# Kernel tuning notes

Hardware: AMD Instinct MI355X
Metric: run time of the kernel (lower is better)

Reference implementation:

```python
import jax, jax.numpy as jnp
import numpy as np
import math

D_MODEL = 1024
NUM_HEADS = 16
D_FF = 4096
EPS = 1e-5
BATCH = 2
SEQ = 2048


def _trunc_normal(key, shape, std):
    # truncated normal on [-3std, 3std], matching nn.init.trunc_normal_
    return std * jax.random.truncated_normal(key, -3.0, 3.0, shape, dtype=jnp.float32)


def setup_inputs() -> dict:
    key = jax.random.key(0)
    ks = jax.random.split(key, 8)
    x = jax.random.normal(ks[0], (BATCH, SEQ, D_MODEL), dtype=jnp.float32)
    std_dd = math.sqrt(2.0 / (D_MODEL + D_MODEL))
    std_up = math.sqrt(2.0 / (D_MODEL + D_FF))
    # Linear stores W as [out_features, in_features]; forward does x @ W.T
    W_q = _trunc_normal(ks[1], (D_MODEL, D_MODEL), std_dd)
    W_k = _trunc_normal(ks[2], (D_MODEL, D_MODEL), std_dd)
    W_v = _trunc_normal(ks[3], (D_MODEL, D_MODEL), std_dd)
    W_o = _trunc_normal(ks[4], (D_MODEL, D_MODEL), std_dd)
    W1 = _trunc_normal(ks[5], (D_FF, D_MODEL), std_up)
    W2 = _trunc_normal(ks[6], (D_MODEL, D_FF), std_up)
    ln1_w = jnp.ones((D_MODEL,), jnp.float32)
    ln1_b = jnp.zeros((D_MODEL,), jnp.float32)
    ln2_w = jnp.ones((D_MODEL,), jnp.float32)
    ln2_b = jnp.zeros((D_MODEL,), jnp.float32)
    return {"x": x, "W_q": W_q, "W_k": W_k, "W_v": W_v, "W_o": W_o,
            "W1": W1, "W2": W2,
            "ln1_w": ln1_w, "ln1_b": ln1_b, "ln2_w": ln2_w, "ln2_b": ln2_b}


def _layernorm(x, w, b):
    xf = x.astype(jnp.float32)
    mean = xf.mean(axis=-1, keepdims=True)
    var = jnp.mean((xf - mean) ** 2, axis=-1, keepdims=True)
    xn = (xf - mean) / jnp.sqrt(var + EPS)
    return (xn * w.astype(jnp.float32) + b.astype(jnp.float32)).astype(x.dtype)


def _attention(x, W_q, W_k, W_v, W_o):
    B, S, D = x.shape
    H, dk = NUM_HEADS, D // NUM_HEADS
    Q = (x @ W_q.T).reshape(B, S, H, dk).transpose(0, 2, 1, 3)  # [B,H,S,dk]
    K = (x @ W_k.T).reshape(B, S, H, dk).transpose(0, 2, 1, 3)
    V = (x @ W_v.T).reshape(B, S, H, dk).transpose(0, 2, 1, 3)
    scores = jnp.einsum('bhqd,bhkd->bhqk', Q, K) / math.sqrt(dk)
    causal = jnp.tril(jnp.ones((S, S), dtype=bool))
    scores = jnp.where(causal, scores, -jnp.inf)
    attn = jax.nn.softmax(scores, axis=-1)
    out = jnp.einsum('bhqk,bhkd->bhqd', attn, V)  # [B,H,S,dk]
    out = out.transpose(0, 2, 1, 3).reshape(B, S, D)
    return out @ W_o.T


def _ffn(x, W1, W2):
    h = x @ W1.T
    h = h * (h > 0)  # ReLU
    return h @ W2.T


def reference(x, W_q, W_k, W_v, W_o, W1, W2, ln1_w, ln1_b, ln2_w, ln2_b):
    x = x + _attention(_layernorm(x, ln1_w, ln1_b), W_q, W_k, W_v, W_o)
    x = x + _ffn(_layernorm(x, ln2_w, ln2_b), W1, W2)
    return x
```

## Files before the change

### kernel.cpp

```cpp
#include <hip/hip_runtime.h>
#include <stdint.h>

typedef unsigned short u16;
typedef unsigned int u32;
typedef __bf16 bf16x8 __attribute__((ext_vector_type(8)));
typedef float f32x4 __attribute__((ext_vector_type(4)));
typedef unsigned short u16x8 __attribute__((ext_vector_type(8)));
typedef unsigned short u16x4 __attribute__((ext_vector_type(4)));
typedef u16x8 u16x8_a __attribute__((may_alias));
typedef u16x4 u16x4_a __attribute__((may_alias));

#define DEV static __device__ __forceinline__

DEV u16 f2bf(float f) {
  unsigned u = __builtin_bit_cast(unsigned, f);
  u += 0x7fffu + ((u >> 16) & 1u);
  return (u16)(u >> 16);
}
DEV bf16x8 ld8(const u16* p) {
  u16x8 v = *(const u16x8_a*)p;
  return __builtin_bit_cast(bf16x8, v);
}
DEV f32x4 vmax4(f32x4 a, f32x4 b) {
  f32x4 r;
  r[0] = fmaxf(a[0], b[0]); r[1] = fmaxf(a[1], b[1]);
  r[2] = fmaxf(a[2], b[2]); r[3] = fmaxf(a[3], b[3]);
  return r;
}
DEV void swz_block(int& bx, int& by) {
  const int gx = gridDim.x;
  const int nwg = gx * gridDim.y;
  int lin = by * gx + bx;
  const int q = nwg >> 3, r = nwg & 7, x = lin & 7, p = lin >> 3;
  lin = (x < r ? x * (q + 1) : r * (q + 1) + (x - r) * q) + p;
  bx = lin % gx; by = lin / gx;
}

#define GL_LDS16(gp, lp)                                                        \
  __builtin_amdgcn_global_load_lds(                                             \
      (const __attribute__((address_space(1))) void*)(gp),                      \
      (__attribute__((address_space(3))) void*)(lp), 16, 0, 0)

#define VMW8 asm volatile("s_waitcnt vmcnt(8)" ::: "memory")
#define VMW4 asm volatile("s_waitcnt vmcnt(4)" ::: "memory")
#define VMW2 asm volatile("s_waitcnt vmcnt(2)" ::: "memory")
#define VMW0 asm volatile("s_waitcnt vmcnt(0)" ::: "memory")
#define BAR  __builtin_amdgcn_s_barrier()

__global__ __launch_bounds__(256) void cvt_k(const float* __restrict__ s,
                                             u16* __restrict__ d, int n4) {
  int i = blockIdx.x * 256 + threadIdx.x;
  if (i < n4) {
    float4 v = ((const float4*)s)[i];
    u16x4 o;
    o[0] = f2bf(v.x); o[1] = f2bf(v.y); o[2] = f2bf(v.z); o[3] = f2bf(v.w);
    *(u16x4_a*)(d + (size_t)i * 4) = o;
  }
}

__global__ __launch_bounds__(256) void ln_k(const float* __restrict__ x,
                                            const float* __restrict__ w,
                                            const float* __restrict__ b,
                                            u16* __restrict__ o) {
  const int row = blockIdx.x, t = threadIdx.x;
  const float4 v = ((const float4*)(x + (size_t)row * 1024))[t];
  float s = v.x + v.y + v.z + v.w;
  float q = v.x * v.x + v.y * v.y + v.z * v.z + v.w * v.w;
#pragma unroll
  for (int m = 1; m < 64; m <<= 1) { s += __shfl_xor(s, m); q += __shfl_xor(q, m); }
  __shared__ float ss[4], qq[4];
  if ((t & 63) == 0) { ss[t >> 6] = s; qq[t >> 6] = q; }
  __syncthreads();
  s = ss[0] + ss[1] + ss[2] + ss[3];
  q = qq[0] + qq[1] + qq[2] + qq[3];
  const float mean = s * (1.f / 1024.f);
  const float var = q * (1.f / 1024.f) - mean * mean;
  const float rstd = rsqrtf(var + 1e-5f);
  const float4 wv = ((const float4*)w)[t];
  const float4 bv = ((const float4*)b)[t];
  u16x4 ov;
  ov[0] = f2bf((v.x - mean) * rstd * wv.x + bv.x);
  ov[1] = f2bf((v.y - mean) * rstd * wv.y + bv.y);
  ov[2] = f2bf((v.z - mean) * rstd * wv.z + bv.z);
  ov[3] = f2bf((v.w - mean) * rstd * wv.w + bv.w);
  *(u16x4_a*)(o + (size_t)row * 1024 + t * 4) = ov;
}

__global__ __launch_bounds__(256) void vtr_k(const u16* __restrict__ qkvV,
                                             u16* __restrict__ vt) {
  __shared__ u16 T[64][65];
  const int st = blockIdx.x, bh = blockIdx.y;
  const int b = bh >> 4, h = bh & 15;
  const int t = threadIdx.x;
  const u16* src = qkvV + ((size_t)(b * 2048 + st * 64)) * 3072 + h * 64;
  const int r = t >> 2, c0 = (t & 3) * 16;
  u16x8 a0 = *(const u16x8_a*)(src + (size_t)r * 3072 + c0);
  u16x8 a1 = *(const u16x8_a*)(src + (size_t)r * 3072 + c0 + 8);
#pragma unroll
  for (int e = 0; e < 8; ++e) { T[r][c0 + e] = a0[e]; T[r][c0 + 8 + e] = a1[e]; }
  __syncthreads();
  const int d = t >> 2, s0 = (t & 3) * 16;
  u16x8 o0, o1;
#pragma unroll
  for (int e = 0; e < 8; ++e) { o0[e] = T[s0 + e][d]; o1[e] = T[s0 + 8 + e][d]; }
  u16* dst = vt + ((size_t)bh * 64 + d) * 2048 + (size_t)st * 64 + s0;
  *(u16x8_a*)dst = o0;
  *(u16x8_a*)(dst + 8) = o1;
}

DEV void stage_op(const u16* __restrict__ G, int K, int kk, u16* lds, int set,
                  int isB, int w, int l) {
#pragma unroll
  for (int i = 0; i < 2; ++i) {
    const int c = i * 8 + w;
    int rb;
    if (!isB) { const int lr = c * 8; rb = (lr < 64 ? lr : lr + 64) + set * 64; }
    else      { rb = (c >> 2) * 64 + set * 32 + (c & 3) * 8; }
    const int row = rb + (l >> 3);
    const int c8 = (l & 7) ^ (row & 7);
    GL_LDS16(G + (size_t)row * K + kk + c8 * 8, lds + rb * 64);
  }
}
DEV void rdA(const u16* as, int wr, int mh, int l15, int l4, bf16x8 af[4][2]) {
#pragma unroll
  for (int f = 0; f < 4; ++f) {
    const int row = wr * 128 + mh * 64 + f * 16 + l15;
#pragma unroll
    for (int ks = 0; ks < 2; ++ks) {
      const int c8 = (ks * 4 + l4) ^ (row & 7);
      af[f][ks] = ld8(as + row * 64 + c8 * 8);
    }
  }
}
DEV void rdB(const u16* bs, int wc, int nh, int l15, int l4, bf16x8 bf_[2][2]) {
#pragma unroll
  for (int g = 0; g < 2; ++g) {
    const int row = wc * 64 + nh * 32 + g * 16 + l15;
#pragma unroll
    for (int ks = 0; ks < 2; ++ks) {
      const int c8 = (ks * 4 + l4) ^ (row & 7);
      bf_[g][ks] = ld8(bs + row * 64 + c8 * 8);
    }
  }
}

#define MFMA16(mh, nh)                                                          \
  __builtin_amdgcn_s_setprio(1);                                                \
  _Pragma("unroll")                                                             \
  for (int f = 0; f < 4; ++f) {                                                 \
    _Pragma("unroll")                                                           \
    for (int g = 0; g < 2; ++g) {                                               \
      f32x4& a_ = acc[(mh) * 4 + f][(nh) * 2 + g];                              \
      a_ = __builtin_amdgcn_mfma_f32_16x16x32_bf16(af[f][0], bfr[g][0], a_, 0, 0, 0); \
      a_ = __builtin_amdgcn_mfma_f32_16x16x32_bf16(af[f][1], bfr[g][1], a_, 0, 0, 0); \
    }                                                                           \
  }                                                                             \
  __builtin_amdgcn_s_setprio(0);

template <int EPI>
__global__ __launch_bounds__(512, 2) void gemm8(const u16* __restrict__ A,
                                                const u16* __restrict__ Bw,
                                                u16* __restrict__ Cp,
                                                int M, int N, int K, int qcols) {
  __shared__ __align__(16) u16 As[2][256 * 64];
  __shared__ __align__(16) u16 Bs[2][256 * 64];
  const int t = threadIdx.x, w = t >> 6, l = t & 63;
  const int l15 = l & 15, l4 = l >> 4;
  const int wr = w >> 2, wc = w & 3;
  int bx = blockIdx.x, by = blockIdx.y;
  swz_block(bx, by);
  const int bm0 = by * 256, bn0 = bx * 256;
  const u16* Ab = A + (size_t)bm0 * K;
  const u16* Bb = Bw + (size_t)bn0 * K;

  f32x4 acc[8][4] = {};
  stage_op(Ab, K, 0, As[0], 0, 0, w, l);
  stage_op(Bb, K, 0, Bs[0], 0, 1, w, l);
  stage_op(Bb, K, 0, Bs[0], 1, 1, w, l);
  stage_op(Ab, K, 0, As[0], 1, 0, w, l);
  VMW4;
  BAR;

  const int nk = K >> 6;
  int cur = 0;
  bf16x8 af[4][2], bfr[2][2];
  for (int kt = 0; kt < nk; ++kt) {
    const int kn = (kt + 1) << 6;
    const bool more = (kt + 1 < nk);
    u16* An = As[cur ^ 1];
    u16* Bn = Bs[cur ^ 1];
    rdA(As[cur], wr, 0, l15, l4, af);
    rdB(Bs[cur], wc, 0, l15, l4, bfr);
    if (more) stage_op(Ab, K, kn, An, 0, 0, w, l);
    BAR;
    MFMA16(0, 0)
    if (more) { VMW4; } else { VMW2; }
    BAR;
    rdB(Bs[cur], wc, 1, l15, l4, bfr);
    if (more) stage_op(Bb, K, kn, Bn, 0, 1, w, l);
    BAR;
    MFMA16(0, 1)
    if (more) { VMW4; } else { VMW0; }
    BAR;
    rdA(As[cur], wr, 1, l15, l4, af);
    if (more) stage_op(Bb, K, kn, Bn, 1, 1, w, l);
    BAR;
    MFMA16(1, 1)
    BAR;
    rdB(Bs[cur], wc, 0, l15, l4, bfr);
    if (more) stage_op(Ab, K, kn, An, 1, 0, w, l);
    BAR;
    MFMA16(1, 0)
    if (more) { VMW4; }
    BAR;
    cur ^= 1;
  }

#pragma unroll
  for (int m = 0; m < 8; ++m) {
    const int row0 = bm0 + wr * 128 + m * 16 + l4 * 4;
#pragma unroll
    for (int n = 0; n < 4; ++n) {
      const int col = bn0 + wc * 64 + n * 16 + l15;
      const float qs = (col < qcols) ? 0.125f : 1.f;
#pragma unroll
      for (int r = 0; r < 4; ++r) {
        float v = acc[m][n][r] * qs;
        if constexpr (EPI == 1) v = v > 0.f ? v : 0.f;
        Cp[(size_t)(row0 + r) * N + col] = f2bf(v);
      }
    }
  }
}

__global__ __launch_bounds__(512, 1) void gemm128(const u16* __restrict__ A,
                                                  const u16* __restrict__ Bw,
                                                  float* __restrict__ C,
                                                  const float* __restrict__ res,
                                                  int M, int N, int K) {
  __shared__ __align__(16) u16 As[3][128 * 64];
  __shared__ __align__(16) u16 Bs[3][128 * 64];
  const int t = threadIdx.x, w = t >> 6, l = t & 63;
  const int l15 = l & 15, l4 = l >> 4;
  const int wr = w >> 2, wc = w & 3;
  int bx = blockIdx.x, by = blockIdx.y;
  swz_block(bx, by);
  const int bm0 = by * 128, bn0 = bx * 128;
  const u16* Ab = A + (size_t)bm0 * K;
  const u16* Bb = Bw + (size_t)bn0 * K;

  auto stg = [&](const u16* __restrict__ G, u16* lds, int kk) {
#pragma unroll
    for (int i = 0; i < 2; ++i) {
      const int c = i * 8 + w;
      const int row = c * 8 + (l >> 3);
      const int c8 = (l & 7) ^ (row & 7);
      GL_LDS16(G + (size_t)row * K + kk + c8 * 8, lds + c * 512);
    }
  };

  f32x4 acc[4][2] = {};
  stg(Ab, As[0], 0);  stg(Bb, Bs[0], 0);
  stg(Ab, As[1], 64); stg(Bb, Bs[1], 64);
  const int nk = K >> 6;
  for (int kt = 0; kt < nk; ++kt) {
    const int cur = kt % 3;
    if (kt + 2 < nk) {
      const int nxt = (kt + 2) % 3;
      const int kk = (kt + 2) << 6;
      stg(Ab, As[nxt], kk);
      stg(Bb, Bs[nxt], kk);
    }
    const int rem = nk - 1 - kt;
    if (rem >= 2) { VMW8; } else if (rem == 1) { VMW4; } else { VMW0; }
    BAR;
    bf16x8 af[4][2], bfr[2][2];
#pragma unroll
    for (int f = 0; f < 4; ++f) {
      const int row = wr * 64 + f * 16 + l15;
#pragma unroll
      for (int ks = 0; ks < 2; ++ks)
        af[f][ks] = ld8(&As[cur][row * 64 + (((ks * 4 + l4) ^ (row & 7)) * 8)]);
    }
#pragma unroll
    for (int g = 0; g < 2; ++g) {
      const int row = wc * 32 + g * 16 + l15;
#pragma unroll
      for (int ks = 0; ks < 2; ++ks)
        bfr[g][ks] = ld8(&Bs[cur][row * 64 + (((ks * 4 + l4) ^ (row & 7)) * 8)]);
    }
    __builtin_amdgcn_s_setprio(1);
#pragma unroll
    for (int f = 0; f < 4; ++f)
#pragma unroll
      for (int g = 0; g < 2; ++g) {
        acc[f][g] = __builtin_amdgcn_mfma_f32_16x16x32_bf16(af[f][0], bfr[g][0], acc[f][g], 0, 0, 0);
        acc[f][g] = __builtin_amdgcn_mfma_f32_16x16x32_bf16(af[f][1], bfr[g][1], acc[f][g], 0, 0, 0);
      }
    __builtin_amdgcn_s_setprio(0);
    BAR;
  }

#pragma unroll
  for (int f = 0; f < 4; ++f) {
    const int row0 = bm0 + wr * 64 + f * 16 + l4 * 4;
#pragma unroll
    for (int g = 0; g < 2; ++g) {
      const int col = bn0 + wc * 32 + g * 16 + l15;
#pragma unroll
      for (int r = 0; r < 4; ++r) {
        const size_t idx = (size_t)(row0 + r) * N + col;
        C[idx] = res[idx] + acc[f][g][r];
      }
    }
  }
}

__global__ __launch_bounds__(256) void attn_k(const u16* __restrict__ Qm,
                                              const u16* __restrict__ Km,
                                              const u16* __restrict__ vt,
                                              u16* __restrict__ Om) {
  const int S = 2048, D = 1024, ldq = 3072;
  int p = blockIdx.x, bh = blockIdx.y;
  swz_block(p, bh);
  const int bb = bh >> 4, h = bh & 15;
  const int t = threadIdx.x, w = t >> 6, l = t & 63, l15 = l & 15, l4 = l >> 4;
  const float NEGINF = -__builtin_inff();

  __shared__ __align__(16) u16 Ksm[2][64 * 64];
  __shared__ __align__(16) u16 Vsm[2][64 * 64];
  __shared__ __align__(16) u32 Psm[4][16 * 32];

  const u16* Qb = Qm + (size_t)bb * S * ldq + h * 64;
  const u16* Kb = Km + (size_t)bb * S * ldq + h * 64;
  const u16* Vtb = vt + (size_t)bh * 64 * 2048;

  auto stageKV = [&](int j, int buf) {
    const int k0 = j * 64;
#pragma unroll
    for (int i = 0; i < 2; ++i) {
      const int s = t + i * 256;
      const int row = s >> 3;
      const int colE = ((s & 7) ^ (row & 7)) * 8;
      GL_LDS16(Kb + (size_t)(k0 + row) * ldq + colE, &Ksm[buf][(s >> 6) * 512]);
      GL_LDS16(Vtb + (size_t)row * 2048 + k0 + colE, &Vsm[buf][(s >> 6) * 512]);
    }
  };

  u32* Pw = &Psm[w][0];
  const u16* Pu = (const u16*)Pw;
  const int h7 = l15 & 7;

  for (int half = 0; half < 2; ++half) {
    const int bx = half ? (31 - p) : p;
    const int q0 = bx * 64;
    __syncthreads();
    stageKV(0, 0);

    bf16x8 qf[2];
    const int qq = q0 + w * 16 + l15;
#pragma unroll
    for (int c = 0; c < 2; ++c) qf[c] = ld8(Qb + (size_t)qq * ldq + c * 32 + l4 * 8);

    f32x4 accT[4] = {};
    float mrow = NEGINF, lrow = 0.f;
    int cur = 0;

    for (int j = 0; j <= bx; ++j) {
      __syncthreads();
      if (j < bx) stageKV(j + 1, cur ^ 1);

      f32x4 sv[4] = {};
      __builtin_amdgcn_s_setprio(1);
#pragma unroll
      for (int c = 0; c < 2; ++c) {
#pragma unroll
        for (int nf = 0; nf < 4; ++nf) {
          const int row = nf * 16 + l15;
          bf16x8 kf = ld8(&Ksm[cur][row * 64 + ((c * 32 + l4 * 8) ^ ((row & 7) * 8))]);
          sv[nf] = __builtin_amdgcn_mfma_f32_16x16x32_bf16(kf, qf[c], sv[nf], 0, 0, 0);
        }
      }
      __builtin_amdgcn_s_setprio(0);

      if (j == bx) {
        const int k0 = j * 64;
#pragma unroll
        for (int nf = 0; nf < 4; ++nf) {
          const int kb = k0 + nf * 16 + l4 * 4;
#pragma unroll
          for (int r = 0; r < 4; ++r)
            if (kb + r > qq) sv[nf][r] = NEGINF;
        }
      }

      f32x4 m4 = vmax4(vmax4(sv[0], sv[1]), vmax4(sv[2], sv[3]));
      float mt = fmaxf(fmaxf(m4[0], m4[1]), fmaxf(m4[2], m4[3]));
      mt = fmaxf(mt, __shfl_xor(mt, 16));
      mt = fmaxf(mt, __shfl_xor(mt, 32));
      const bool skip = __all(mt - mrow <= 8.f);
      const float mnew = skip ? mrow : fmaxf(mrow, mt);
      if (!skip) {
        const float sf = __expf(mrow - mnew);
        lrow *= sf;
#pragma unroll
        for (int nf = 0; nf < 4; ++nf) accT[nf] *= sf;
        mrow = mnew;
      }
#pragma unroll
      for (int nf = 0; nf < 4; ++nf)
#pragma unroll
        for (int r = 0; r < 4; ++r) sv[nf][r] = __expf(sv[nf][r] - mnew);
      f32x4 s4 = (sv[0] + sv[1]) + (sv[2] + sv[3]);
      float ps = (s4[0] + s4[1]) + (s4[2] + s4[3]);
      ps += __shfl_xor(ps, 16);
      ps += __shfl_xor(ps, 32);
      lrow += ps;

#pragma unroll
      for (int nf = 0; nf < 4; ++nf) {
        u32 lo, hi;
        asm("v_cvt_pk_bf16_f32 %0, %1, %2" : "=v"(lo) : "v"(sv[nf][0]), "v"(sv[nf][1]));
        asm("v_cvt_pk_bf16_f32 %0, %1, %2" : "=v"(hi) : "v"(sv[nf][2]), "v"(sv[nf][3]));
        const int kw4 = (nf * 2 + (l4 >> 1)) ^ h7;
        const int base = l15 * 32 + kw4 * 4 + (l4 & 1) * 2;
        Pw[base] = lo;
        Pw[base + 1] = hi;
      }

      __builtin_amdgcn_s_setprio(1);
#pragma unroll
      for (int c = 0; c < 2; ++c) {
        bf16x8 pf = ld8(Pu + l15 * 64 + ((c * 4 + l4) ^ h7) * 8);
#pragma unroll
        for (int nf = 0; nf < 4; ++nf) {
          const int row = nf * 16 + l15;
          bf16x8 vf = ld8(&Vsm[cur][row * 64 + ((c * 32 + l4 * 8) ^ ((row & 7) * 8))]);
          accT[nf] = __builtin_amdgcn_mfma_f32_16x16x32_bf16(vf, pf, accT[nf], 0, 0, 0);
        }
      }
      __builtin_amdgcn_s_setprio(0);
      cur ^= 1;
    }

    const float inv = 1.f / lrow;
    u16* orow = Om + ((size_t)bb * S + qq) * D + h * 64;
#pragma unroll
    for (int nf = 0; nf < 4; ++nf) {
      u16x4 ov;
#pragma unroll
      for (int r = 0; r < 4; ++r) ov[r] = f2bf(accT[nf][r] * inv);
      *(u16x4_a*)(orow + nf * 16 + l4 * 4) = ov;
    }
  }
}

extern "C" void kernel_launch(void* const* d_in, const int* in_sizes, int n_in,
                              void* d_out, int out_size, void* d_ws, size_t ws_size,
                              hipStream_t stream) {
  (void)in_sizes; (void)n_in; (void)out_size; (void)ws_size;
  const float* x    = (const float*)d_in[0];
  const float* W_q  = (const float*)d_in[1];
  const float* W_k  = (const float*)d_in[2];
  const float* W_v  = (const float*)d_in[3];
  const float* W_o  = (const float*)d_in[4];
  const float* W1   = (const float*)d_in[5];
  const float* W2   = (const float*)d_in[6];
  const float* ln1w = (const float*)d_in[7];
  const float* ln1b = (const float*)d_in[8];
  const float* ln2w = (const float*)d_in[9];
  const float* ln2b = (const float*)d_in[10];

  const size_t MB = 1ull << 20;
  char* W = (char*)d_ws;
  u16* wqkv  = (u16*)(W + 0);
  u16* wo    = (u16*)(W + 6 * MB);
  u16* w1b   = (u16*)(W + 8 * MB);
  u16* w2b   = (u16*)(W + 16 * MB);
  u16* xn1   = (u16*)(W + 24 * MB);
  u16* qkv   = (u16*)(W + 32 * MB);
  u16* attnb = (u16*)(W + 56 * MB);
  u16* vt    = (u16*)(W + 64 * MB);
  u16* xn2   = (u16*)(W + 64 * MB);
  u16* hbuf  = (u16*)(W + 24 * MB);
  float* x2  = (float*)d_out;

  auto cvt = [&](const float* s, u16* d, int n) {
    int n4 = n >> 2;
    cvt_k<<<dim3((n4 + 255) / 256), dim3(256), 0, stream>>>(s, d, n4);
  };
  cvt(W_q, wqkv, 1 << 20);
  cvt(W_k, wqkv + (1 << 20), 1 << 20);
  cvt(W_v, wqkv + (2 << 20), 1 << 20);
  cvt(W_o, wo, 1 << 20);
  cvt(W1, w1b, 4 << 20);
  cvt(W2, w2b, 4 << 20);

  ln_k<<<dim3(4096), dim3(256), 0, stream>>>(x, ln1w, ln1b, xn1);
  gemm8<0><<<dim3(12, 16), dim3(512), 0, stream>>>(xn1, wqkv, qkv, 4096, 3072, 1024, 1024);
  vtr_k<<<dim3(32, 32), dim3(256), 0, stream>>>(qkv + 2048, vt);
  attn_k<<<dim3(16, 32), dim3(256), 0, stream>>>(qkv, qkv + 1024, vt, attnb);
  gemm128<<<dim3(8, 32), dim3(512), 0, stream>>>(attnb, wo, x2, x, 4096, 1024, 1024);
  ln_k<<<dim3(4096), dim3(256), 0, stream>>>(x2, ln2w, ln2b, xn2);
  gemm8<1><<<dim3(16, 16), dim3(512), 0, stream>>>(xn2, w1b, hbuf, 4096, 4096, 1024, 0);
  gemm128<<<dim3(8, 32), dim3(512), 0, stream>>>(hbuf, w2b, x2, x2, 4096, 1024, 4096);
}
```

Before: 246.0 us.

## Load B operand directly to registers in gemm128, staging only A through LDS

In the residual-add 128x128 GEMM, the B (weight) tile is no longer staged through LDS. Each wave now loads its own B fragments straight from global memory into registers, using a triple-buffered register rotation that the loop unrolls by three. Only A keeps the LDS pipeline, which halves LDS use and the LDS reads per k-step. The cost is more VGPRs and redundant global B loads across the two wave rows, and the vmcnt wait counts are retuned to cover the extra outstanding loads.

```diff
diff --git a/kernel.cpp b/kernel.cpp
--- a/kernel.cpp
+++ b/kernel.cpp
@@ -41,11 +41,13 @@
       (const __attribute__((address_space(1))) void*)(gp),                      \
       (__attribute__((address_space(3))) void*)(lp), 16, 0, 0)
 
-#define VMW8 asm volatile("s_waitcnt vmcnt(8)" ::: "memory")
-#define VMW4 asm volatile("s_waitcnt vmcnt(4)" ::: "memory")
-#define VMW2 asm volatile("s_waitcnt vmcnt(2)" ::: "memory")
-#define VMW0 asm volatile("s_waitcnt vmcnt(0)" ::: "memory")
-#define BAR  __builtin_amdgcn_s_barrier()
+#define VMW12 asm volatile("s_waitcnt vmcnt(12)" ::: "memory")
+#define VMW8  asm volatile("s_waitcnt vmcnt(8)" ::: "memory")
+#define VMW6  asm volatile("s_waitcnt vmcnt(6)" ::: "memory")
+#define VMW4  asm volatile("s_waitcnt vmcnt(4)" ::: "memory")
+#define VMW2  asm volatile("s_waitcnt vmcnt(2)" ::: "memory")
+#define VMW0  asm volatile("s_waitcnt vmcnt(0)" ::: "memory")
+#define BAR   __builtin_amdgcn_s_barrier()
 
 __global__ __launch_bounds__(256) void cvt_k(const float* __restrict__ s,
                                              u16* __restrict__ d, int n4) {
@@ -239,7 +241,6 @@
                                                   const float* __restrict__ res,
                                                   int M, int N, int K) {
   __shared__ __align__(16) u16 As[3][128 * 64];
-  __shared__ __align__(16) u16 Bs[3][128 * 64];
   const int t = threadIdx.x, w = t >> 6, l = t & 63;
   const int l15 = l & 15, l4 = l >> 4;
   const int wr = w >> 2, wc = w & 3;
@@ -249,57 +250,68 @@
   const u16* Ab = A + (size_t)bm0 * K;
   const u16* Bb = Bw + (size_t)bn0 * K;
 
-  auto stg = [&](const u16* __restrict__ G, u16* lds, int kk) {
+  auto stgA = [&](int buf, int kk) {
 #pragma unroll
     for (int i = 0; i < 2; ++i) {
       const int c = i * 8 + w;
       const int row = c * 8 + (l >> 3);
       const int c8 = (l & 7) ^ (row & 7);
-      GL_LDS16(G + (size_t)row * K + kk + c8 * 8, lds + c * 512);
+      GL_LDS16(Ab + (size_t)row * K + kk + c8 * 8, &As[buf][c * 512]);
     }
   };
-
-  f32x4 acc[4][2] = {};
-  stg(Ab, As[0], 0);  stg(Bb, Bs[0], 0);
-  stg(Ab, As[1], 64); stg(Bb, Bs[1], 64);
-  const int nk = K >> 6;
-  for (int kt = 0; kt < nk; ++kt) {
-    const int cur = kt % 3;
-    if (kt + 2 < nk) {
-      const int nxt = (kt + 2) % 3;
-      const int kk = (kt + 2) << 6;
-      stg(Ab, As[nxt], kk);
-      stg(Bb, Bs[nxt], kk);
-    }
-    const int rem = nk - 1 - kt;
-    if (rem >= 2) { VMW8; } else if (rem == 1) { VMW4; } else { VMW0; }
-    BAR;
-    bf16x8 af[4][2], bfr[2][2];
+  auto ldB = [&](bf16x8 (&bf_)[2][2], int kk) {
+#pragma unroll
+    for (int g = 0; g < 2; ++g) {
+      const int row = wc * 32 + g * 16 + l15;
+#pragma unroll
+      for (int ks = 0; ks < 2; ++ks)
+        bf_[g][ks] = ld8(Bb + (size_t)row * K + kk + (ks * 4 + l4) * 8);
+    }
+  };
+  auto rdAf = [&](bf16x8 (&af)[4][2], int cb) {
 #pragma unroll
     for (int f = 0; f < 4; ++f) {
       const int row = wr * 64 + f * 16 + l15;
 #pragma unroll
       for (int ks = 0; ks < 2; ++ks)
-        af[f][ks] = ld8(&As[cur][row * 64 + (((ks * 4 + l4) ^ (row & 7)) * 8)]);
-    }
-#pragma unroll
-    for (int g = 0; g < 2; ++g) {
-      const int row = wc * 32 + g * 16 + l15;
-#pragma unroll
-      for (int ks = 0; ks < 2; ++ks)
-        bfr[g][ks] = ld8(&Bs[cur][row * 64 + (((ks * 4 + l4) ^ (row & 7)) * 8)]);
-    }
-    __builtin_amdgcn_s_setprio(1);
-#pragma unroll
-    for (int f = 0; f < 4; ++f)
-#pragma unroll
-      for (int g = 0; g < 2; ++g) {
-        acc[f][g] = __builtin_amdgcn_mfma_f32_16x16x32_bf16(af[f][0], bfr[g][0], acc[f][g], 0, 0, 0);
-        acc[f][g] = __builtin_amdgcn_mfma_f32_16x16x32_bf16(af[f][1], bfr[g][1], acc[f][g], 0, 0, 0);
-      }
-    __builtin_amdgcn_s_setprio(0);
-    BAR;
-  }
+        af[f][ks] = ld8(&As[cb][row * 64 + (((ks * 4 + l4) ^ (row & 7)) * 8)]);
+    }
+  };
+
+  f32x4 acc[4][2] = {};
+  bf16x8 b0[2][2], b1[2][2], b2[2][2];
+  const int nk = K >> 6;
+  stgA(0, 0);  ldB(b0, 0);
+  stgA(1, 64); ldB(b1, 64);
+
+#define G128_STEP(kt_, BUSE, BLOAD)                                            \
+  {                                                                            \
+    const int kt = (kt_);                                                      \
+    if (kt >= nk) break;                                                       \
+    if (kt + 2 < nk) { stgA((kt + 2) % 3, (kt + 2) << 6); ldB(BLOAD, (kt + 2) << 6); } \
+    if (kt + 2 < nk) { VMW12; } else if (kt + 1 < nk) { VMW6; } else { VMW0; } \
+    BAR;                                                                       \
+    bf16x8 af[4][2];                                                           \
+    rdAf(af, kt % 3);                                                          \
+    __builtin_amdgcn_s_setprio(1);                                             \
+    _Pragma("unroll")                                                          \
+    for (int f = 0; f < 4; ++f) {                                              \
+      _Pragma("unroll")                                                        \
+      for (int g = 0; g < 2; ++g) {                                            \
+        acc[f][g] = __builtin_amdgcn_mfma_f32_16x16x32_bf16(af[f][0], BUSE[g][0], acc[f][g], 0, 0, 0); \
+        acc[f][g] = __builtin_amdgcn_mfma_f32_16x16x32_bf16(af[f][1], BUSE[g][1], acc[f][g], 0, 0, 0); \
+      }                                                                        \
+    }                                                                          \
+    __builtin_amdgcn_s_setprio(0);                                             \
+    BAR;                                                                       \
+  }
+
+  for (int ktb = 0;; ktb += 3) {
+    G128_STEP(ktb + 0, b0, b2)
+    G128_STEP(ktb + 1, b1, b0)
+    G128_STEP(ktb + 2, b2, b1)
+  }
+#undef G128_STEP
 
 #pragma unroll
   for (int f = 0; f < 4; ++f) {
```

New measurement: 265.6 us. 8.0% more time.

## Split-K the FFN down-projection GEMM with separate partial-sum reduction

Applied to the files above, without the earlier changes.

The W2 GEMM (K=4096) is split into two K-chunks across a z grid dimension, doubling the block count. The first chunk writes residual plus partial result to the output, and the second writes to a workspace buffer. A new elementwise kernel then adds the partial into the output. This aims to raise occupancy and parallelism, at the cost of extra global memory traffic and an extra launch for the reduction.

```diff
diff --git a/kernel.cpp b/kernel.cpp
--- a/kernel.cpp
+++ b/kernel.cpp
@@ -55,6 +55,17 @@
     u16x4 o;
     o[0] = f2bf(v.x); o[1] = f2bf(v.y); o[2] = f2bf(v.z); o[3] = f2bf(v.w);
     *(u16x4_a*)(d + (size_t)i * 4) = o;
+  }
+}
+
+__global__ __launch_bounds__(256) void red_k(const float* __restrict__ p,
+                                             float* __restrict__ d, int n4) {
+  int i = blockIdx.x * 256 + threadIdx.x;
+  if (i < n4) {
+    float4 a = ((const float4*)d)[i];
+    float4 b = ((const float4*)p)[i];
+    a.x += b.x; a.y += b.y; a.z += b.z; a.w += b.w;
+    ((float4*)d)[i] = a;
   }
 }
 
@@ -316,6 +327,88 @@
   }
 }
 
+__global__ __launch_bounds__(512, 4) void gemm128s(const u16* __restrict__ A,
+                                                   const u16* __restrict__ Bw,
+                                                   float* __restrict__ C,
+                                                   float* __restrict__ P,
+                                                   const float* __restrict__ res,
+                                                   int M, int N, int K, int Kc) {
+  __shared__ __align__(16) u16 As[2][128 * 64];
+  __shared__ __align__(16) u16 Bs[2][128 * 64];
+  const int t = threadIdx.x, w = t >> 6, l = t & 63;
+  const int l15 = l & 15, l4 = l >> 4;
+  const int wr = w >> 2, wc = w & 3;
+  int bx = blockIdx.x, by = blockIdx.y;
+  swz_block(bx, by);
+  const int kz = blockIdx.z;
+  const int bm0 = by * 128, bn0 = bx * 128;
+  const u16* Ab = A + (size_t)bm0 * K + (size_t)kz * Kc;
+  const u16* Bb = Bw + (size_t)bn0 * K + (size_t)kz * Kc;
+
+  auto stg = [&](const u16* __restrict__ G, u16* lds, int kk) {
+#pragma unroll
+    for (int i = 0; i < 2; ++i) {
+      const int c = i * 8 + w;
+      const int row = c * 8 + (l >> 3);
+      const int c8 = (l & 7) ^ (row & 7);
+      GL_LDS16(G + (size_t)row * K + kk + c8 * 8, lds + c * 512);
+    }
+  };
+
+  f32x4 acc[4][2] = {};
+  stg(Ab, As[0], 0); stg(Bb, Bs[0], 0);
+  const int nk = Kc >> 6;
+  int cur = 0;
+  for (int kt = 0; kt < nk; ++kt) {
+    __syncthreads();
+    if (kt + 1 < nk) {
+      stg(Ab, As[cur ^ 1], (kt + 1) << 6);
+      stg(Bb, Bs[cur ^ 1], (kt + 1) << 6);
+    }
+    bf16x8 af[4][2], bfr[2][2];
+#pragma unroll
+    for (int f = 0; f < 4; ++f) {
+      const int row = wr * 64 + f * 16 + l15;
+#pragma unroll
+      for (int ks = 0; ks < 2; ++ks)
+        af[f][ks] = ld8(&As[cur][row * 64 + (((ks * 4 + l4) ^ (row & 7)) * 8)]);
+    }
+#pragma unroll
+    for (int g = 0; g < 2; ++g) {
+      const int row = wc * 32 + g * 16 + l15;
+#pragma unroll
+      for (int ks = 0; ks < 2; ++ks)
+        bfr[g][ks] = ld8(&Bs[cur][row * 64 + (((ks * 4 + l4) ^ (row & 7)) * 8)]);
+    }
+    __builtin_amdgcn_s_setprio(1);
+#pragma unroll
+    for (int f = 0; f < 4; ++f)
+#pragma unroll
+      for (int g = 0; g < 2; ++g) {
+        acc[f][g] = __builtin_amdgcn_mfma_f32_16x16x32_bf16(af[f][0], bfr[g][0], acc[f][g], 0, 0, 0);
+        acc[f][g] = __builtin_amdgcn_mfma_f32_16x16x32_bf16(af[f][1], bfr[g][1], acc[f][g], 0, 0, 0);
+      }
+    __builtin_amdgcn_s_setprio(0);
+    __syncthreads();
+    cur ^= 1;
+  }
+
+#pragma unroll
+  for (int f = 0; f < 4; ++f) {
+    const int row0 = bm0 + wr * 64 + f * 16 + l4 * 4;
+#pragma unroll
+    for (int g = 0; g < 2; ++g) {
+      const int col = bn0 + wc * 32 + g * 16 + l15;
+#pragma unroll
+      for (int r = 0; r < 4; ++r) {
+        const size_t idx = (size_t)(row0 + r) * N + col;
+        if (kz == 0) C[idx] = res[idx] + acc[f][g][r];
+        else         P[idx] = acc[f][g][r];
+      }
+    }
+  }
+}
+
 __global__ __launch_bounds__(256) void attn_k(const u16* __restrict__ Qm,
                                               const u16* __restrict__ Km,
                                               const u16* __restrict__ vt,
@@ -483,6 +576,7 @@
   u16* vt    = (u16*)(W + 64 * MB);
   u16* xn2   = (u16*)(W + 64 * MB);
   u16* hbuf  = (u16*)(W + 24 * MB);
+  float* fpart = (float*)(W + 56 * MB);
   float* x2  = (float*)d_out;
 
   auto cvt = [&](const float* s, u16* d, int n) {
@@ -503,5 +597,7 @@
   gemm128<<<dim3(8, 32), dim3(512), 0, stream>>>(attnb, wo, x2, x, 4096, 1024, 1024);
   ln_k<<<dim3(4096), dim3(256), 0, stream>>>(x2, ln2w, ln2b, xn2);
   gemm8<1><<<dim3(16, 16), dim3(512), 0, stream>>>(xn2, w1b, hbuf, 4096, 4096, 1024, 0);
-  gemm128<<<dim3(8, 32), dim3(512), 0, stream>>>(hbuf, w2b, x2, x2, 4096, 1024, 4096);
-}
+  gemm128s<<<dim3(8, 32, 2), dim3(512), 0, stream>>>(hbuf, w2b, x2, fpart, x2,
+                                                     4096, 1024, 4096, 2048);
+  red_k<<<dim3(4096), dim3(256), 0, stream>>>(fpart, x2, 1 << 20);
+}
```

Result: faster. 232.7 us (-5.4%).
